# Performance work log

Measured on AMD Instinct MI355X. Metric: run time of the kernel, lower is better.

The kernel has to match this reference:

```python
import jax, jax.numpy as jnp
import numpy as np

# ---- static configuration (matches init_kwargs / input_specs) ----
B, N = 4, 128            # images, proposals per image
C = 256                  # feature channels (in_channels)
HF, WF = 23, 30          # feature map size (input 736x960 / 32)
PH, PW = 7, 7            # pooled_size
SCALE = 1.0 / 32.0       # scale_factor
HIMG, WIMG = HF * 32, WF * 32
KH = HF // PH + 2        # max rows any pooling bin can span
KW = WF // PW + 2        # max cols any pooling bin can span
HID, OUT = 256, 5
NEG = -1e30


def _roi_pool_one(f, box):
    """Quantized ROI max pooling for one proposal.
    f: (C, HF, WF) feature map; box: (4,) [x1,y1,x2,y2] in feature coords.
    Returns (C, PH, PW)."""
    box = jax.lax.stop_gradient(box)  # indices are non-differentiable
    x1 = jnp.clip(jnp.floor(box[0]).astype(jnp.int32), 0, WF - 1)
    y1 = jnp.clip(jnp.floor(box[1]).astype(jnp.int32), 0, HF - 1)
    roi_w = jnp.clip(jnp.ceil(box[2]).astype(jnp.int32) - x1, 1, WF)
    roi_h = jnp.clip(jnp.ceil(box[3]).astype(jnp.int32) - y1, 1, HF)
    ph = jnp.arange(PH)
    pw = jnp.arange(PW)
    hs = y1 + (ph * roi_h) // PH                       # bin row starts (PH,)
    he = y1 + ((ph + 1) * roi_h + PH - 1) // PH        # bin row ends (ceil)
    ws = x1 + (pw * roi_w) // PW
    we = x1 + ((pw + 1) * roi_w + PW - 1) // PW
    hidx = hs[:, None] + jnp.arange(KH)[None, :]       # (PH, KH)
    hval = (hidx < he[:, None]) & (hidx < HF)
    widx = ws[:, None] + jnp.arange(KW)[None, :]       # (PW, KW)
    wval = (widx < we[:, None]) & (widx < WF)
    rows = f[:, jnp.clip(hidx, 0, HF - 1), :]          # (C, PH, KH, WF) gather
    rmax = jnp.max(jnp.where(hval[None, :, :, None], rows, NEG), axis=2)  # (C, PH, WF)
    cols = rmax[:, :, jnp.clip(widx, 0, WF - 1)]       # (C, PH, PW, KW) gather
    return jnp.max(jnp.where(wval[None, None], cols, NEG), axis=3)        # (C, PH, PW)


# vmap over proposals, then over images: (B,C,HF,WF),(B,N,4) -> (B,N,C,PH,PW)
_roi_pool = jax.vmap(jax.vmap(_roi_pool_one, in_axes=(None, 0)), in_axes=(0, 0))


def setup_inputs() -> dict:
    key = jax.random.key(0)
    ks = jax.random.split(key, 8)
    features = jax.random.normal(ks[0], (B, C, HF, WF), jnp.float32)
    # valid proposals in image coordinates (min box side ~32 px)
    x1 = jax.random.uniform(ks[1], (B, N)) * (WIMG - 32.0)
    y1 = jax.random.uniform(ks[2], (B, N)) * (HIMG - 32.0)
    x2 = x1 + 32.0 + jax.random.uniform(ks[3], (B, N)) * (WIMG - 32.0 - x1)
    y2 = y1 + 32.0 + jax.random.uniform(ks[4], (B, N)) * (HIMG - 32.0 - y1)
    conf = jax.random.normal(ks[5], (B, N))
    proposals = jnp.stack([x1, y1, x2, y2, conf], axis=-1)  # (B, N, 5)
    W1 = jax.random.normal(ks[6], (HID, C * PH * PW), jnp.float32) * 0.01
    b1 = jnp.zeros((HID,), jnp.float32)
    W2 = jax.random.normal(ks[7], (OUT, HID), jnp.float32) * 0.01
    b2 = jnp.zeros((OUT,), jnp.float32)
    return {"features": features, "proposals": proposals,
            "W1": W1, "b1": b1, "W2": W2, "b2": b2}


def reference(features, proposals, W1, b1, W2, b2):
    boxes_feat = proposals[..., :4] * SCALE                 # image -> feature coords
    pooled = _roi_pool(features, boxes_feat)                # (B, N, C, PH, PW)
    flat = pooled.reshape(B, N, C * PH * PW)
    h = jax.nn.relu(jnp.einsum('bnf,hf->bnh', flat, W1) + b1)
    out = jnp.einsum('bnh,oh->bno', h, W2) + b2             # (B, N, 5)
    refined_boxes = proposals[..., :4] + out[..., :4]
    refined_conf = jax.nn.sigmoid(proposals[..., 4:5] + out[..., 4:5])
    return jnp.concatenate([refined_boxes, refined_conf], axis=-1)  # (B, N, 5)
```

## Files before the change

### kernel.cpp

```cpp
#include <hip/hip_runtime.h>
#include <math.h>

#define Bq 4
#define Nq 128
#define Cq 256
#define HFq 23
#define WFq 30
#define PHq 7
#define PWq 7
#define HIDq 256
#define OUTq 5
#define Fq (Cq*PHq*PWq)
#define Mq (Bq*Nq)
#define HWq (HFq*WFq)
#define SCALEq (1.0f/32.0f)
#define NEGq (-1e30f)
#define KHq 5
#define KWq 6
#define SPLITK 14
#define KCH (Fq/SPLITK)
#define KSTEPS (KCH/32)

typedef float f32x4 __attribute__((ext_vector_type(4)));
typedef __bf16 bf16x8 __attribute__((ext_vector_type(8)));

__device__ __forceinline__ unsigned short f2b(float f) {
    unsigned int u = __float_as_uint(f);
    unsigned int r = (u + 0x7FFFu + ((u >> 16) & 1u)) >> 16;
    return (unsigned short)r;
}

__global__ __launch_bounds__(256) void k_transpose(const float* __restrict__ feat,
                                                   float* __restrict__ ft) {
    __shared__ float t[32][33];
    int bb = blockIdx.z;
    const float* src = feat + (size_t)bb * Cq * HWq;
    float* dst = ft + (size_t)bb * HWq * Cq;
    int x0 = blockIdx.x * 32;
    int c0 = blockIdx.y * 32;
    int tx = threadIdx.x, ty = threadIdx.y;
#pragma unroll
    for (int i = 0; i < 4; ++i) {
        int c = c0 + ty + i * 8;
        int x = x0 + tx;
        if (x < HWq) t[ty + i * 8][tx] = src[(size_t)c * HWq + x];
    }
    __syncthreads();
#pragma unroll
    for (int i = 0; i < 4; ++i) {
        int x = x0 + ty + i * 8;
        int c = c0 + tx;
        if (x < HWq) dst[(size_t)x * Cq + c] = t[tx][ty + i * 8];
    }
}

__global__ __launch_bounds__(256) void k_w1perm(const float* __restrict__ W1,
                                                unsigned short* __restrict__ w1p) {
    __shared__ __align__(16) unsigned short s[Fq];
    int j = blockIdx.x;
    const float4* src = (const float4*)(W1 + (size_t)j * Fq);
    for (int i = threadIdx.x; i < Fq / 4; i += 256) {
        float4 v = src[i];
        ushort4 o;
        o.x = f2b(v.x); o.y = f2b(v.y); o.z = f2b(v.z); o.w = f2b(v.w);
        ((ushort4*)s)[i] = o;
    }
    __syncthreads();
    uint4* dst = (uint4*)(w1p + (size_t)j * Fq);
    for (int i = threadIdx.x; i < Fq / 8; i += 256) {
        int base = i * 8;
        int cell = base >> 8;
        int c0 = base & 255;
        unsigned short tmp[8];
#pragma unroll
        for (int u = 0; u < 8; ++u) tmp[u] = s[(c0 + u) * 49 + cell];
        dst[i] = *(const uint4*)tmp;
    }
}

__global__ __launch_bounds__(256) void k_pool(const float* __restrict__ ft,
                                              const float* __restrict__ props,
                                              unsigned short* __restrict__ pooled) {
    int wave = threadIdx.x >> 6;
    int lane = threadIdx.x & 63;
    int g = blockIdx.y * 4 + wave;
    int m = blockIdx.x;
    int b = m >> 7;
    const float* pr = props + (size_t)m * 5;
    float b0 = pr[0] * SCALEq, b1v = pr[1] * SCALEq;
    float b2v = pr[2] * SCALEq, b3v = pr[3] * SCALEq;
    int x1 = min(max((int)floorf(b0), 0), WFq - 1);
    int y1 = min(max((int)floorf(b1v), 0), HFq - 1);
    int rw = min(max((int)ceilf(b2v) - x1, 1), WFq);
    int rh = min(max((int)ceilf(b3v) - y1, 1), HFq);
    const float* ftb = ft + (size_t)b * HWq * Cq + lane * 4;
    unsigned short* pm = pooled + (size_t)m * Fq + lane * 4;

    for (int cell = g; cell < PHq * PWq; cell += 8) {
        int ph = cell / 7;
        int pw = cell - ph * 7;
        int hs = y1 + (ph * rh) / PHq;
        int he = min(y1 + ((ph + 1) * rh + PHq - 1) / PHq, HFq);
        int ws = x1 + (pw * rw) / PWq;
        int we = min(x1 + ((pw + 1) * rw + PWq - 1) / PWq, WFq);
        f32x4 acc = {NEGq, NEGq, NEGq, NEGq};
#pragma unroll
        for (int kh = 0; kh < KHq; ++kh) {
            if (hs + kh < he) {
                const float* rowp = ftb + (size_t)((hs + kh) * WFq) * Cq;
#pragma unroll
                for (int kw = 0; kw < KWq; ++kw) {
                    if (ws + kw < we) {
                        f32x4 v = *(const f32x4*)(rowp + (size_t)(ws + kw) * Cq);
                        acc.x = fmaxf(acc.x, v.x);
                        acc.y = fmaxf(acc.y, v.y);
                        acc.z = fmaxf(acc.z, v.z);
                        acc.w = fmaxf(acc.w, v.w);
                    }
                }
            }
        }
        ushort4 o;
        o.x = f2b(acc.x); o.y = f2b(acc.y); o.z = f2b(acc.z); o.w = f2b(acc.w);
        *(ushort4*)(pm + (size_t)cell * Cq) = o;
    }
}

__global__ __launch_bounds__(256) void k_gemm1(const unsigned short* __restrict__ pooled,
                                               const unsigned short* __restrict__ w1p,
                                               float* __restrict__ part) {
    __shared__ __align__(16) unsigned short As[64 * 32];
    __shared__ __align__(16) unsigned short Bs[64 * 32];
    int m0 = blockIdx.x * 64;
    int j0 = blockIdx.y * 64;
    int kz = blockIdx.z;
    int tid = threadIdx.x;
    int r = tid >> 2, qq = tid & 3;
    const uint4* ap = (const uint4*)(pooled + (size_t)(m0 + r) * Fq + (size_t)kz * KCH + qq * 8);
    const uint4* bp = (const uint4*)(w1p + (size_t)(j0 + r) * Fq + (size_t)kz * KCH + qq * 8);
    int lane = tid & 63, wv = tid >> 6;
    int q = lane >> 4, mr = lane & 15;
    f32x4 acc0 = {0.f, 0.f, 0.f, 0.f};
    f32x4 acc1 = {0.f, 0.f, 0.f, 0.f};
    f32x4 acc2 = {0.f, 0.f, 0.f, 0.f};
    f32x4 acc3 = {0.f, 0.f, 0.f, 0.f};
    const bf16x8* afp = (const bf16x8*)(As + (wv * 16 + mr) * 32 + q * 8);
    const bf16x8* bfp0 = (const bf16x8*)(Bs + (0 + mr) * 32 + q * 8);
    const bf16x8* bfp1 = (const bf16x8*)(Bs + (16 + mr) * 32 + q * 8);
    const bf16x8* bfp2 = (const bf16x8*)(Bs + (32 + mr) * 32 + q * 8);
    const bf16x8* bfp3 = (const bf16x8*)(Bs + (48 + mr) * 32 + q * 8);
    uint4* asw = (uint4*)(As + r * 32 + qq * 8);
    uint4* bsw = (uint4*)(Bs + r * 32 + qq * 8);
    uint4 av = ap[0];
    uint4 bv = bp[0];
    for (int s = 0; s < KSTEPS; ++s) {
        __syncthreads();
        *asw = av;
        *bsw = bv;
        __syncthreads();
        if (s + 1 < KSTEPS) {
            av = ap[(s + 1) * 4];
            bv = bp[(s + 1) * 4];
        }
        bf16x8 a = *afp;
        acc0 = __builtin_amdgcn_mfma_f32_16x16x32_bf16(a, *bfp0, acc0, 0, 0, 0);
        acc1 = __builtin_amdgcn_mfma_f32_16x16x32_bf16(a, *bfp1, acc1, 0, 0, 0);
        acc2 = __builtin_amdgcn_mfma_f32_16x16x32_bf16(a, *bfp2, acc2, 0, 0, 0);
        acc3 = __builtin_amdgcn_mfma_f32_16x16x32_bf16(a, *bfp3, acc3, 0, 0, 0);
    }
    float* pbase = part + (size_t)kz * Mq * HIDq;
    int mb = m0 + wv * 16 + q * 4;
    int jj = j0 + mr;
#pragma unroll
    for (int r2 = 0; r2 < 4; ++r2) {
        float* row = pbase + (size_t)(mb + r2) * HIDq + jj;
        row[0]  = acc0[r2];
        row[16] = acc1[r2];
        row[32] = acc2[r2];
        row[48] = acc3[r2];
    }
}

__global__ __launch_bounds__(256) void k_reduce(const float* __restrict__ part,
                                                const float* __restrict__ b1,
                                                float* __restrict__ h) {
    int m = blockIdx.x, j = threadIdx.x;
    float s = 0.f;
#pragma unroll
    for (int z = 0; z < SPLITK; ++z) s += part[((size_t)z * Mq + m) * HIDq + j];
    s += b1[j];
    h[(size_t)m * HIDq + j] = fmaxf(s, 0.f);
}

__global__ __launch_bounds__(256) void k_final(const float* __restrict__ h,
                                               const float* __restrict__ W2,
                                               const float* __restrict__ b2,
                                               const float* __restrict__ props,
                                               float* __restrict__ out) {
    __shared__ float red[OUTq][4];
    int m = blockIdx.x, j = threadIdx.x;
    float hv = h[(size_t)m * HIDq + j];
    float p[OUTq];
#pragma unroll
    for (int o = 0; o < OUTq; ++o) p[o] = hv * W2[(size_t)o * HIDq + j];
    int lane = j & 63, wid = j >> 6;
#pragma unroll
    for (int o = 0; o < OUTq; ++o) {
        float v = p[o];
        v += __shfl_xor(v, 1);
        v += __shfl_xor(v, 2);
        v += __shfl_xor(v, 4);
        v += __shfl_xor(v, 8);
        v += __shfl_xor(v, 16);
        v += __shfl_xor(v, 32);
        if (lane == 0) red[o][wid] = v;
    }
    __syncthreads();
    if (j < OUTq) {
        float s = red[j][0] + red[j][1] + red[j][2] + red[j][3] + b2[j];
        float pv = props[(size_t)m * 5 + j];
        float r;
        if (j < 4) r = pv + s;
        else r = 1.f / (1.f + expf(-(pv + s)));
        out[(size_t)m * 5 + j] = r;
    }
}

extern "C" void kernel_launch(void* const* d_in, const int* in_sizes, int n_in,
                              void* d_out, int out_size, void* d_ws, size_t ws_size,
                              hipStream_t stream) {
    const float* feat  = (const float*)d_in[0];
    const float* props = (const float*)d_in[1];
    const float* W1    = (const float*)d_in[2];
    const float* b1    = (const float*)d_in[3];
    const float* W2    = (const float*)d_in[4];
    const float* b2    = (const float*)d_in[5];
    float* out = (float*)d_out;

    char* ws = (char*)d_ws;
    float* ft              = (float*)(ws);
    unsigned short* w1p    = (unsigned short*)(ws + 2826240);
    unsigned short* pooled = (unsigned short*)(ws + 9248768);
    float* part            = (float*)(ws + 22093824);
    float* h               = (float*)(ws + 29433856);

    k_transpose<<<dim3(22, 8, 4), dim3(32, 8), 0, stream>>>(feat, ft);
    k_w1perm<<<HIDq, 256, 0, stream>>>(W1, w1p);
    k_pool<<<dim3(Mq, 2), 256, 0, stream>>>(ft, props, pooled);
    k_gemm1<<<dim3(8, 4, SPLITK), 256, 0, stream>>>(pooled, w1p, part);
    k_reduce<<<Mq, 256, 0, stream>>>(part, b1, h);
    k_final<<<Mq, 256, 0, stream>>>(h, W2, b2, props, out);
}
```

Before: 128.7 us.

## Merge prep kernels, use atomic split-K reduction, and fold bias/ReLU into tail

The transpose, W1 bf16 permutation and zeroing of h now run as one kernel launch, with block index ranges selecting the role. The split-K GEMM now accumulates directly into h with atomicAdd, which removes the partial buffer and the separate reduce kernel. Bias and ReLU are applied in the final kernel instead. This cuts launches from six to four and drops the partial-sum round trip through memory. In exchange it adds contention on the float atomics and makes the summation order nondeterministic.

After: 126.5 us. Within noise of the previous version (-1.7%).

```diff
diff --git a/kernel.cpp b/kernel.cpp
--- a/kernel.cpp
+++ b/kernel.cpp
@@ -30,51 +30,62 @@
     return (unsigned short)r;
 }
 
-__global__ __launch_bounds__(256) void k_transpose(const float* __restrict__ feat,
-                                                   float* __restrict__ ft) {
-    __shared__ float t[32][33];
-    int bb = blockIdx.z;
-    const float* src = feat + (size_t)bb * Cq * HWq;
-    float* dst = ft + (size_t)bb * HWq * Cq;
-    int x0 = blockIdx.x * 32;
-    int c0 = blockIdx.y * 32;
-    int tx = threadIdx.x, ty = threadIdx.y;
-#pragma unroll
-    for (int i = 0; i < 4; ++i) {
-        int c = c0 + ty + i * 8;
-        int x = x0 + tx;
-        if (x < HWq) t[ty + i * 8][tx] = src[(size_t)c * HWq + x];
-    }
-    __syncthreads();
-#pragma unroll
-    for (int i = 0; i < 4; ++i) {
-        int x = x0 + ty + i * 8;
-        int c = c0 + tx;
-        if (x < HWq) dst[(size_t)x * Cq + c] = t[tx][ty + i * 8];
-    }
-}
-
-__global__ __launch_bounds__(256) void k_w1perm(const float* __restrict__ W1,
-                                                unsigned short* __restrict__ w1p) {
-    __shared__ __align__(16) unsigned short s[Fq];
-    int j = blockIdx.x;
-    const float4* src = (const float4*)(W1 + (size_t)j * Fq);
-    for (int i = threadIdx.x; i < Fq / 4; i += 256) {
-        float4 v = src[i];
-        ushort4 o;
-        o.x = f2b(v.x); o.y = f2b(v.y); o.z = f2b(v.z); o.w = f2b(v.w);
-        ((ushort4*)s)[i] = o;
-    }
-    __syncthreads();
-    uint4* dst = (uint4*)(w1p + (size_t)j * Fq);
-    for (int i = threadIdx.x; i < Fq / 8; i += 256) {
-        int base = i * 8;
-        int cell = base >> 8;
-        int c0 = base & 255;
-        unsigned short tmp[8];
-#pragma unroll
-        for (int u = 0; u < 8; ++u) tmp[u] = s[(c0 + u) * 49 + cell];
-        dst[i] = *(const uint4*)tmp;
+__global__ __launch_bounds__(256) void k_prep(const float* __restrict__ feat,
+                                              float* __restrict__ ft,
+                                              const float* __restrict__ W1,
+                                              unsigned short* __restrict__ w1p,
+                                              float* __restrict__ h) {
+    __shared__ __align__(16) unsigned short smem[Fq];
+    int bid = blockIdx.x;
+    int tid = threadIdx.x;
+    if (bid < 704) {
+        float (*t)[33] = (float (*)[33])smem;
+        int bb  = bid / 176;
+        int rem = bid % 176;
+        int x0 = (rem % 22) * 32;
+        int c0 = (rem / 22) * 32;
+        int tx = tid & 31, ty = tid >> 5;
+        const float* src = feat + (size_t)bb * Cq * HWq;
+        float* dst = ft + (size_t)bb * HWq * Cq;
+#pragma unroll
+        for (int i = 0; i < 4; ++i) {
+            int c = c0 + ty + i * 8;
+            int x = x0 + tx;
+            if (x < HWq) t[ty + i * 8][tx] = src[(size_t)c * HWq + x];
+        }
+        __syncthreads();
+#pragma unroll
+        for (int i = 0; i < 4; ++i) {
+            int x = x0 + ty + i * 8;
+            int c = c0 + tx;
+            if (x < HWq) dst[(size_t)x * Cq + c] = t[tx][ty + i * 8];
+        }
+    } else if (bid < 960) {
+        int j = bid - 704;
+        const float4* src = (const float4*)(W1 + (size_t)j * Fq);
+        for (int i = tid; i < Fq / 4; i += 256) {
+            float4 v = src[i];
+            ushort4 o;
+            o.x = f2b(v.x); o.y = f2b(v.y); o.z = f2b(v.z); o.w = f2b(v.w);
+            ((ushort4*)smem)[i] = o;
+        }
+        __syncthreads();
+        uint4* dst = (uint4*)(w1p + (size_t)j * Fq);
+        for (int i = tid; i < Fq / 8; i += 256) {
+            int base = i * 8;
+            int cell = base >> 8;
+            int c0v = base & 255;
+            unsigned short tmp[8];
+#pragma unroll
+            for (int u = 0; u < 8; ++u) tmp[u] = smem[(c0v + u) * 49 + cell];
+            dst[i] = *(const uint4*)tmp;
+        }
+    } else {
+        f32x4* h4 = (f32x4*)h;
+        int base = (bid - 960) * 4096;
+        f32x4 z = {0.f, 0.f, 0.f, 0.f};
+#pragma unroll
+        for (int u = 0; u < 16; ++u) h4[base + u * 256 + tid] = z;
     }
 }
 
@@ -128,7 +139,7 @@
 
 __global__ __launch_bounds__(256) void k_gemm1(const unsigned short* __restrict__ pooled,
                                                const unsigned short* __restrict__ w1p,
-                                               float* __restrict__ part) {
+                                               float* __restrict__ h) {
     __shared__ __align__(16) unsigned short As[64 * 32];
     __shared__ __align__(16) unsigned short Bs[64 * 32];
     int m0 = blockIdx.x * 64;
@@ -168,38 +179,27 @@
         acc2 = __builtin_amdgcn_mfma_f32_16x16x32_bf16(a, *bfp2, acc2, 0, 0, 0);
         acc3 = __builtin_amdgcn_mfma_f32_16x16x32_bf16(a, *bfp3, acc3, 0, 0, 0);
     }
-    float* pbase = part + (size_t)kz * Mq * HIDq;
     int mb = m0 + wv * 16 + q * 4;
     int jj = j0 + mr;
 #pragma unroll
     for (int r2 = 0; r2 < 4; ++r2) {
-        float* row = pbase + (size_t)(mb + r2) * HIDq + jj;
-        row[0]  = acc0[r2];
-        row[16] = acc1[r2];
-        row[32] = acc2[r2];
-        row[48] = acc3[r2];
-    }
-}
-
-__global__ __launch_bounds__(256) void k_reduce(const float* __restrict__ part,
-                                                const float* __restrict__ b1,
-                                                float* __restrict__ h) {
-    int m = blockIdx.x, j = threadIdx.x;
-    float s = 0.f;
-#pragma unroll
-    for (int z = 0; z < SPLITK; ++z) s += part[((size_t)z * Mq + m) * HIDq + j];
-    s += b1[j];
-    h[(size_t)m * HIDq + j] = fmaxf(s, 0.f);
-}
-
-__global__ __launch_bounds__(256) void k_final(const float* __restrict__ h,
-                                               const float* __restrict__ W2,
-                                               const float* __restrict__ b2,
-                                               const float* __restrict__ props,
-                                               float* __restrict__ out) {
+        float* row = h + (size_t)(mb + r2) * HIDq + jj;
+        atomicAdd(row + 0,  acc0[r2]);
+        atomicAdd(row + 16, acc1[r2]);
+        atomicAdd(row + 32, acc2[r2]);
+        atomicAdd(row + 48, acc3[r2]);
+    }
+}
+
+__global__ __launch_bounds__(256) void k_tail(const float* __restrict__ h,
+                                              const float* __restrict__ b1,
+                                              const float* __restrict__ W2,
+                                              const float* __restrict__ b2,
+                                              const float* __restrict__ props,
+                                              float* __restrict__ out) {
     __shared__ float red[OUTq][4];
     int m = blockIdx.x, j = threadIdx.x;
-    float hv = h[(size_t)m * HIDq + j];
+    float hv = fmaxf(h[(size_t)m * HIDq + j] + b1[j], 0.f);
     float p[OUTq];
 #pragma unroll
     for (int o = 0; o < OUTq; ++o) p[o] = hv * W2[(size_t)o * HIDq + j];
@@ -241,13 +241,10 @@
     float* ft              = (float*)(ws);
     unsigned short* w1p    = (unsigned short*)(ws + 2826240);
     unsigned short* pooled = (unsigned short*)(ws + 9248768);
-    float* part            = (float*)(ws + 22093824);
-    float* h               = (float*)(ws + 29433856);
-
-    k_transpose<<<dim3(22, 8, 4), dim3(32, 8), 0, stream>>>(feat, ft);
-    k_w1perm<<<HIDq, 256, 0, stream>>>(W1, w1p);
+    float* h               = (float*)(ws + 22093824);
+
+    k_prep<<<968, 256, 0, stream>>>(feat, ft, W1, w1p, h);
     k_pool<<<dim3(Mq, 2), 256, 0, stream>>>(ft, props, pooled);
-    k_gemm1<<<dim3(8, 4, SPLITK), 256, 0, stream>>>(pooled, w1p, part);
-    k_reduce<<<Mq, 256, 0, stream>>>(part, b1, h);
-    k_final<<<Mq, 256, 0, stream>>>(h, W2, b2, props, out);
-}
+    k_gemm1<<<dim3(8, 4, SPLITK), 256, 0, stream>>>(pooled, w1p, h);
+    k_tail<<<Mq, 256, 0, stream>>>(h, b1, W2, b2, props, out);
+}
```
